# Kernel optimization log

Hardware: AMD Instinct MI355X
Metric: run time of the kernel (lower is better)

The kernel has to match this reference:

```python
import jax, jax.numpy as jnp
import numpy as np
from math import sqrt

DIM, RANK = 1024, 32
B, S = 4, 4096

def setup_inputs() -> dict:
    key = jax.random.key(0)
    kx, kq, kk, kv = jax.random.split(key, 4)
    # xavier_uniform bounds
    bq = sqrt(6.0 / (RANK + DIM))
    bv = sqrt(6.0 / (DIM + DIM))
    return {
        "x": jax.random.normal(kx, (B, S, DIM), dtype=jnp.float32),
        "Q": jax.random.uniform(kq, (RANK, DIM), jnp.float32, -bq, bq),
        "K": jax.random.uniform(kk, (RANK, DIM), jnp.float32, -bq, bq),
        "VO": jax.random.uniform(kv, (DIM, DIM), jnp.float32, -bv, bv),
    }

def reference(x, Q, K, VO):
    d = x.shape[-1]
    # low-rank projections: [b,t,r] each (avoid materializing QK^T [d,d] or 4-way einsum blowup)
    xq = jnp.einsum('btd,rd->btr', x, Q)
    xk = jnp.einsum('bud,rd->bur', x, K)
    scores = jnp.einsum('btr,bur->btu', xq, xk) / sqrt(d)
    attn = jax.nn.softmax(scores, axis=2)
    # value aggregation then output projection
    ctx = jnp.einsum('btu,bud->btd', attn, x)
    return jnp.einsum('btd,de->bte', ctx, VO)
```

## Files before the change

### kernel.cpp

```cpp
#include <hip/hip_runtime.h>
#include <hip/hip_bf16.h>

#define DIM  1024
#define RANK 32
#define BATCH 4
#define SEQ  4096
#define MTOT (BATCH * SEQ)

typedef short bf16x8 __attribute__((ext_vector_type(8)));
typedef float f32x4 __attribute__((ext_vector_type(4)));
typedef float f32x16 __attribute__((ext_vector_type(16)));
typedef unsigned short ushort8v __attribute__((ext_vector_type(8)));
typedef unsigned int uint2v __attribute__((ext_vector_type(2)));

__device__ inline unsigned short f2bf(float f) {
    union { float f; unsigned int u; } v; v.f = f;
    return (unsigned short)((v.u + 0x7FFFu + ((v.u >> 16) & 1u)) >> 16);
}

__device__ inline unsigned int pk_bf16(float a, float b) {
    __hip_bfloat162 h = __float22bfloat162_rn(make_float2(a, b));
    unsigned int u; __builtin_memcpy(&u, &h, 4);
    return u;
}

__device__ inline void gl_lds16(const unsigned short* g, unsigned short* l) {
    __builtin_amdgcn_global_load_lds(
        (const __attribute__((address_space(1))) unsigned int*)g,
        (__attribute__((address_space(3))) unsigned int*)l, 16, 0, 0);
}

__global__ __launch_bounds__(256) void k_cvt_qk(const float* __restrict__ Q,
                                                const float* __restrict__ K,
                                                unsigned short* __restrict__ wqk) {
    int i = blockIdx.x * 256 + threadIdx.x;
    int row = i >> 10, col = i & 1023;
    const float SC = 0.045084220027779984f;
    float v = (row < RANK) ? Q[row * DIM + col] * SC : K[(row - RANK) * DIM + col];
    wqk[i] = f2bf(v);
}

__global__ __launch_bounds__(256) void k_transpose_cvt(const float* __restrict__ in,
                                                       unsigned short* __restrict__ out,
                                                       int R, int C) {
    __shared__ float tile[64][65];
    const int tid = threadIdx.x;
    const int c0 = blockIdx.x * 64, r0 = blockIdx.y * 64;
    {
        int c = (tid & 15) * 4;
#pragma unroll
        for (int i = 0; i < 4; ++i) {
            int r = (tid >> 4) + i * 16;
            f32x4 v = *(const f32x4*)(in + (size_t)(r0 + r) * C + c0 + c);
            tile[r][c + 0] = v[0]; tile[r][c + 1] = v[1];
            tile[r][c + 2] = v[2]; tile[r][c + 3] = v[3];
        }
    }
    __syncthreads();
    {
        int r = (tid & 15) * 4;
#pragma unroll
        for (int i = 0; i < 4; ++i) {
            int c = (tid >> 4) + i * 16;
            unsigned short o0 = f2bf(tile[r + 0][c]), o1 = f2bf(tile[r + 1][c]);
            unsigned short o2 = f2bf(tile[r + 2][c]), o3 = f2bf(tile[r + 3][c]);
            unsigned short* p = out + (size_t)(c0 + c) * R + r0 + r;
            p[0] = o0; p[1] = o1; p[2] = o2; p[3] = o3;
        }
    }
}

__global__ __launch_bounds__(256) void k_xbf(const float* __restrict__ x,
                                             unsigned short* __restrict__ xbf) {
    size_t i = ((size_t)blockIdx.x * 256 + threadIdx.x) * 8;
    f32x4 v0 = *(const f32x4*)(x + i);
    f32x4 v1 = *(const f32x4*)(x + i + 4);
    ushort8v o;
    o[0] = f2bf(v0[0]); o[1] = f2bf(v0[1]); o[2] = f2bf(v0[2]); o[3] = f2bf(v0[3]);
    o[4] = f2bf(v1[0]); o[5] = f2bf(v1[1]); o[6] = f2bf(v1[2]); o[7] = f2bf(v1[3]);
    *(ushort8v*)(xbf + i) = o;
}

__global__ __launch_bounds__(256) void k_proj(const unsigned short* __restrict__ xbf,
                                              const unsigned short* __restrict__ wqk,
                                              unsigned short* __restrict__ xqk) {
    __shared__ __align__(16) unsigned short a_lds[128 * 32];
    __shared__ __align__(16) unsigned short w_lds[64 * 32];
    const int tid = threadIdx.x;
    const int w = tid >> 6, lane = tid & 63, l15 = lane & 15, quad = lane >> 4;
    const int wm = w & 1, wn = w >> 1;
    const int rowbase = blockIdx.x * 128;

    f32x4 acc[4][2];
#pragma unroll
    for (int mt = 0; mt < 4; ++mt)
#pragma unroll
        for (int nt = 0; nt < 2; ++nt) acc[mt][nt] = (f32x4){0.f, 0.f, 0.f, 0.f};

    const unsigned short* Ab = xbf + (size_t)(rowbase + w * 32 + (lane >> 2)) * DIM + (lane & 3) * 8;
    const unsigned short* Wb = wqk + (size_t)(w * 16 + (lane >> 2)) * DIM + (lane & 3) * 8;

    for (int k0 = 0; k0 < DIM; k0 += 32) {
        gl_lds16(Ab + k0, &a_lds[(w * 32) * 32]);
        gl_lds16(Ab + (size_t)16 * DIM + k0, &a_lds[(w * 32 + 16) * 32]);
        gl_lds16(Wb + k0, &w_lds[(w * 16) * 32]);
        __syncthreads();
        bf16x8 am[4], bn[2];
#pragma unroll
        for (int mt = 0; mt < 4; ++mt)
            am[mt] = *(const bf16x8*)&a_lds[(wm * 64 + mt * 16 + l15) * 32 + quad * 8];
#pragma unroll
        for (int nt = 0; nt < 2; ++nt)
            bn[nt] = *(const bf16x8*)&w_lds[(wn * 32 + nt * 16 + l15) * 32 + quad * 8];
#pragma unroll
        for (int mt = 0; mt < 4; ++mt)
#pragma unroll
            for (int nt = 0; nt < 2; ++nt)
                acc[mt][nt] = __builtin_amdgcn_mfma_f32_16x16x32_bf16(am[mt], bn[nt], acc[mt][nt], 0, 0, 0);
        __syncthreads();
    }
#pragma unroll
    for (int mt = 0; mt < 4; ++mt)
#pragma unroll
        for (int nt = 0; nt < 2; ++nt)
#pragma unroll
            for (int r = 0; r < 4; ++r) {
                int grow = rowbase + wm * 64 + mt * 16 + quad * 4 + r;
                xqk[(size_t)grow * 64 + wn * 32 + nt * 16 + l15] = f2bf(acc[mt][nt][r]);
            }
}

__global__ __launch_bounds__(512, 4) void k_xvo(const unsigned short* __restrict__ vot,
                                                const unsigned short* __restrict__ xbf,
                                                unsigned short* __restrict__ xvoT) {
    __shared__ __align__(16) unsigned short a_lds[128 * 64];
    __shared__ __align__(16) unsigned short b_lds[256 * 64];
    const int tid = threadIdx.x;
    const int w = tid >> 6, lane = tid & 63, l31 = lane & 31, half = lane >> 5;
    const int wm = w & 1, wn = w >> 1;
    const int ubase = blockIdx.x * 256;
    const int ebase = blockIdx.y * 128;
    const int b = blockIdx.z;

    f32x16 acc[2][2];
#pragma unroll
    for (int at = 0; at < 2; ++at)
#pragma unroll
        for (int bt = 0; bt < 2; ++bt)
#pragma unroll
            for (int i = 0; i < 16; ++i) acc[at][bt][i] = 0.f;

    const int sub = lane >> 3;
    const int g = (lane & 7) ^ (sub & 7);
    const int Ra = w * 16 + sub;
    const int Rb = w * 32 + sub;
    const unsigned short* Ap = vot + (size_t)(ebase + Ra) * DIM + g * 8;
    const unsigned short* Bp = xbf + (size_t)(b * SEQ + ubase + Rb) * DIM + g * 8;

    for (int k0 = 0; k0 < DIM; k0 += 64) {
#pragma unroll
        for (int c = 0; c < 2; ++c)
            gl_lds16(Ap + (size_t)(c * 8) * DIM + k0, &a_lds[(w * 16 + c * 8) * 64]);
#pragma unroll
        for (int c = 0; c < 4; ++c)
            gl_lds16(Bp + (size_t)(c * 8) * DIM + k0, &b_lds[(w * 32 + c * 8) * 64]);
        __syncthreads();

        const int abase = (wm * 64 + l31) * 64;
        const int bbase = (wn * 64 + l31) * 64;
#pragma unroll
        for (int ks = 0; ks < 4; ++ks) {
            const int soff = ((ks * 2 + half) ^ (l31 & 7)) * 8;
            bf16x8 a0 = *(const bf16x8*)&a_lds[abase + soff];
            bf16x8 a1 = *(const bf16x8*)&a_lds[abase + 2048 + soff];
            bf16x8 b0 = *(const bf16x8*)&b_lds[bbase + soff];
            bf16x8 b1 = *(const bf16x8*)&b_lds[bbase + 2048 + soff];
            acc[0][0] = __builtin_amdgcn_mfma_f32_32x32x16_bf16(a0, b0, acc[0][0], 0, 0, 0);
            acc[0][1] = __builtin_amdgcn_mfma_f32_32x32x16_bf16(a0, b1, acc[0][1], 0, 0, 0);
            acc[1][0] = __builtin_amdgcn_mfma_f32_32x32x16_bf16(a1, b0, acc[1][0], 0, 0, 0);
            acc[1][1] = __builtin_amdgcn_mfma_f32_32x32x16_bf16(a1, b1, acc[1][1], 0, 0, 0);
        }
        __syncthreads();
    }
#pragma unroll
    for (int at = 0; at < 2; ++at)
#pragma unroll
        for (int bt = 0; bt < 2; ++bt)
#pragma unroll
            for (int reg = 0; reg < 16; ++reg) {
                int lr = wm * 64 + at * 32 + (reg & 3) + 8 * (reg >> 2) + 4 * half;
                int u = ubase + wn * 64 + bt * 32 + l31;
                xvoT[(size_t)(b * DIM + ebase + lr) * SEQ + u] = f2bf(acc[at][bt][reg]);
            }
}

__global__ __launch_bounds__(512, 4) void k_spv(const unsigned short* __restrict__ xqk,
                                                const unsigned short* __restrict__ xvoT,
                                                float* __restrict__ out) {
    __shared__ __align__(16) unsigned short p_lds[128 * 64];
    __shared__ __align__(16) unsigned short b_lds[256 * 64];
    __shared__ float denp[8][32];
    __shared__ float rden[128];
    const int tid = threadIdx.x;
    const int w = tid >> 6, lane = tid & 63, l31 = lane & 31, half = lane >> 5;
    const int wm = w & 1, wn = w >> 1;
    const int uu = w & 1, qq = w >> 1;

    const int p = blockIdx.x;
    const int xcd = p & 7, t0 = p >> 3;
    const int rowtile = xcd * 16 + (t0 >> 2);
    const int etile = t0 & 3;
    const int rowbase = rowtile * 128;
    const int ebase = etile * 256;
    const int b = rowbase >> 12;

    const unsigned short* xqp = xqk + (size_t)(rowbase + qq * 32 + l31) * 64 + half * 8;
    const bf16x8 bq0 = *(const bf16x8*)(xqp);
    const bf16x8 bq1 = *(const bf16x8*)(xqp + 16);

    const unsigned short* xkp = xqk + (size_t)(b * SEQ + uu * 32 + l31) * 64 + 32 + half * 8;

    f32x16 acc[2][2];
#pragma unroll
    for (int at = 0; at < 2; ++at)
#pragma unroll
        for (int bt = 0; bt < 2; ++bt)
#pragma unroll
            for (int i = 0; i < 16; ++i) acc[at][bt][i] = 0.f;

    const int sub = lane >> 3;
    const int g8 = (lane & 7) ^ (sub & 7);
    const unsigned short* Bp = xvoT + (size_t)(b * DIM + ebase + w * 32 + sub) * SEQ + g8 * 8;
    auto stageB = [&](int k0) {
#pragma unroll
        for (int c = 0; c < 4; ++c)
            gl_lds16(Bp + (size_t)(c * 8) * SEQ + k0, &b_lds[(w * 32 + c * 8) * 64]);
    };

    const int NT = SEQ / 64;
    float dacc = 0.f;
    const int pbase = (qq * 32 + l31) * 64 + half * 4;

    stageB(0);
    bf16x8 kA0 = *(const bf16x8*)(xkp);
    bf16x8 kA1 = *(const bf16x8*)(xkp + 16);
    bf16x8 kB0, kB1;

    for (int t = 0; t < NT; ++t) {
        f32x16 sc;
#pragma unroll
        for (int i = 0; i < 16; ++i) sc[i] = 0.f;
        sc = __builtin_amdgcn_mfma_f32_32x32x16_bf16(kA0, bq0, sc, 0, 0, 0);
        sc = __builtin_amdgcn_mfma_f32_32x32x16_bf16(kA1, bq1, sc, 0, 0, 0);
#pragma unroll
        for (int g = 0; g < 4; ++g) {
            float e0 = exp2f(sc[4 * g + 0]), e1 = exp2f(sc[4 * g + 1]);
            float e2 = exp2f(sc[4 * g + 2]), e3 = exp2f(sc[4 * g + 3]);
            dacc += (e0 + e1) + (e2 + e3);
            uint2v dw; dw[0] = pk_bf16(e0, e1); dw[1] = pk_bf16(e2, e3);
            *(uint2v*)&p_lds[pbase + (((uu * 4 + g) ^ (l31 & 7)) * 8)] = dw;
        }
        asm volatile("s_waitcnt lgkmcnt(0)" ::: "memory");
        asm volatile("s_waitcnt vmcnt(0)" ::: "memory");
        __builtin_amdgcn_s_barrier();
        asm volatile("" ::: "memory");

        {
            const unsigned short* nx = xkp + (size_t)((t + 1 < NT) ? (t + 1) : t) * 4096;
            kB0 = *(const bf16x8*)(nx);
            kB1 = *(const bf16x8*)(nx + 16);
        }

        const int abase = (wm * 64 + l31) * 64;
        const int bbase = (wn * 64 + l31) * 64;
        __builtin_amdgcn_s_setprio(1);
#pragma unroll
        for (int ks = 0; ks < 4; ++ks) {
            const int soff = ((ks * 2 + half) ^ (l31 & 7)) * 8;
            bf16x8 a0 = *(const bf16x8*)&p_lds[abase + soff];
            bf16x8 a1 = *(const bf16x8*)&p_lds[abase + 2048 + soff];
            bf16x8 b0 = *(const bf16x8*)&b_lds[bbase + soff];
            bf16x8 b1 = *(const bf16x8*)&b_lds[bbase + 2048 + soff];
            acc[0][0] = __builtin_amdgcn_mfma_f32_32x32x16_bf16(a0, b0, acc[0][0], 0, 0, 0);
            acc[0][1] = __builtin_amdgcn_mfma_f32_32x32x16_bf16(a0, b1, acc[0][1], 0, 0, 0);
            acc[1][0] = __builtin_amdgcn_mfma_f32_32x32x16_bf16(a1, b0, acc[1][0], 0, 0, 0);
            acc[1][1] = __builtin_amdgcn_mfma_f32_32x32x16_bf16(a1, b1, acc[1][1], 0, 0, 0);
        }
        __builtin_amdgcn_s_setprio(0);
        asm volatile("s_waitcnt lgkmcnt(0)" ::: "memory");
        __builtin_amdgcn_s_barrier();
        asm volatile("" ::: "memory");

        if (t + 1 < NT) stageB((t + 1) * 64);
        kA0 = kB0; kA1 = kB1;
    }

    dacc += __shfl_xor(dacc, 32);
    if (half == 0) denp[w][l31] = dacc;
    __syncthreads();
    if (tid < 128)
        rden[tid] = 1.0f / (denp[(tid >> 5) * 2][tid & 31] + denp[(tid >> 5) * 2 + 1][tid & 31]);
    __syncthreads();

#pragma unroll
    for (int at = 0; at < 2; ++at)
#pragma unroll
        for (int bt = 0; bt < 2; ++bt)
#pragma unroll
            for (int reg = 0; reg < 16; ++reg) {
                int lr = wm * 64 + at * 32 + (reg & 3) + 8 * (reg >> 2) + 4 * half;
                int e = ebase + wn * 64 + bt * 32 + l31;
                out[(size_t)(rowbase + lr) * DIM + e] = acc[at][bt][reg] * rden[lr];
            }
}

extern "C" void kernel_launch(void* const* d_in, const int* in_sizes, int n_in,
                              void* d_out, int out_size, void* d_ws, size_t ws_size,
                              hipStream_t stream) {
    const float* x  = (const float*)d_in[0];
    const float* Q  = (const float*)d_in[1];
    const float* K  = (const float*)d_in[2];
    const float* VO = (const float*)d_in[3];
    float* out = (float*)d_out;

    char* ws = (char*)d_ws;
    unsigned short* wqk  = (unsigned short*)(ws + 0);
    unsigned short* vot  = (unsigned short*)(ws + 131072);
    unsigned short* xqk  = (unsigned short*)(ws + 2228224);
    unsigned short* xbf  = (unsigned short*)(ws + 4325376);
    unsigned short* xvoT = (unsigned short*)(ws + 37879808);

    k_cvt_qk<<<256, 256, 0, stream>>>(Q, K, wqk);
    k_transpose_cvt<<<dim3(16, 16, 1), 256, 0, stream>>>(VO, vot, 1024, 1024);
    k_xbf<<<8192, 256, 0, stream>>>(x, xbf);
    k_proj<<<128, 256, 0, stream>>>(xbf, wqk, xqk);
    k_xvo<<<dim3(16, 8, BATCH), 512, 0, stream>>>(vot, xbf, xvoT);
    k_spv<<<dim3(512, 1, 1), 512, 0, stream>>>(xqk, xvoT, out);
}
```

Before: 341.9 us.

## Software-pipeline score/exp computation with PV MFMA using double-buffered P tile

Double-buffers the probability tile in LDS so the scores MFMA and exp2 for tile t+1 are computed while the PV MFMAs for tile t run, instead of serially before them. The first tile's scores are computed in a prologue. The s_setprio hints are removed. B staging now waits on vmcnt right after issue and adds a second barrier per iteration, which exposes global-load latency that the old schedule partly hid behind the score computation.

```diff
diff --git a/kernel.cpp b/kernel.cpp
--- a/kernel.cpp
+++ b/kernel.cpp
@@ -197,7 +197,7 @@
 __global__ __launch_bounds__(512, 4) void k_spv(const unsigned short* __restrict__ xqk,
                                                 const unsigned short* __restrict__ xvoT,
                                                 float* __restrict__ out) {
-    __shared__ __align__(16) unsigned short p_lds[128 * 64];
+    __shared__ __align__(16) unsigned short p_lds[2][128 * 64];
     __shared__ __align__(16) unsigned short b_lds[256 * 64];
     __shared__ float denp[8][32];
     __shared__ float rden[128];
@@ -242,43 +242,52 @@
     const int pbase = (qq * 32 + l31) * 64 + half * 4;
 
     stageB(0);
-    bf16x8 kA0 = *(const bf16x8*)(xkp);
-    bf16x8 kA1 = *(const bf16x8*)(xkp + 16);
-    bf16x8 kB0, kB1;
-
-    for (int t = 0; t < NT; ++t) {
+    bf16x8 kCur0 = *(const bf16x8*)(xkp);
+    bf16x8 kCur1 = *(const bf16x8*)(xkp + 16);
+    {
         f32x16 sc;
 #pragma unroll
         for (int i = 0; i < 16; ++i) sc[i] = 0.f;
-        sc = __builtin_amdgcn_mfma_f32_32x32x16_bf16(kA0, bq0, sc, 0, 0, 0);
-        sc = __builtin_amdgcn_mfma_f32_32x32x16_bf16(kA1, bq1, sc, 0, 0, 0);
+        sc = __builtin_amdgcn_mfma_f32_32x32x16_bf16(kCur0, bq0, sc, 0, 0, 0);
+        sc = __builtin_amdgcn_mfma_f32_32x32x16_bf16(kCur1, bq1, sc, 0, 0, 0);
 #pragma unroll
         for (int g = 0; g < 4; ++g) {
             float e0 = exp2f(sc[4 * g + 0]), e1 = exp2f(sc[4 * g + 1]);
             float e2 = exp2f(sc[4 * g + 2]), e3 = exp2f(sc[4 * g + 3]);
             dacc += (e0 + e1) + (e2 + e3);
             uint2v dw; dw[0] = pk_bf16(e0, e1); dw[1] = pk_bf16(e2, e3);
-            *(uint2v*)&p_lds[pbase + (((uu * 4 + g) ^ (l31 & 7)) * 8)] = dw;
-        }
-        asm volatile("s_waitcnt lgkmcnt(0)" ::: "memory");
-        asm volatile("s_waitcnt vmcnt(0)" ::: "memory");
-        __builtin_amdgcn_s_barrier();
-        asm volatile("" ::: "memory");
-
-        {
-            const unsigned short* nx = xkp + (size_t)((t + 1 < NT) ? (t + 1) : t) * 4096;
-            kB0 = *(const bf16x8*)(nx);
-            kB1 = *(const bf16x8*)(nx + 16);
-        }
-
+            *(uint2v*)&p_lds[0][pbase + (((uu * 4 + g) ^ (l31 & 7)) * 8)] = dw;
+        }
+    }
+    {
+        const unsigned short* nx = xkp + 4096;
+        kCur0 = *(const bf16x8*)(nx);
+        kCur1 = *(const bf16x8*)(nx + 16);
+    }
+    asm volatile("s_waitcnt lgkmcnt(0)" ::: "memory");
+    asm volatile("s_waitcnt vmcnt(0)" ::: "memory");
+    __builtin_amdgcn_s_barrier();
+    asm volatile("" ::: "memory");
+
+    bf16x8 kNext0 = kCur0, kNext1 = kCur1;
+    for (int t = 0; t < NT; ++t) {
+        const bool more = (t + 1 < NT);
+        f32x16 sc;
+#pragma unroll
+        for (int i = 0; i < 16; ++i) sc[i] = 0.f;
+        if (more) {
+            sc = __builtin_amdgcn_mfma_f32_32x32x16_bf16(kCur0, bq0, sc, 0, 0, 0);
+            sc = __builtin_amdgcn_mfma_f32_32x32x16_bf16(kCur1, bq1, sc, 0, 0, 0);
+        }
+
+        const unsigned short* pl = p_lds[t & 1];
         const int abase = (wm * 64 + l31) * 64;
         const int bbase = (wn * 64 + l31) * 64;
-        __builtin_amdgcn_s_setprio(1);
 #pragma unroll
         for (int ks = 0; ks < 4; ++ks) {
             const int soff = ((ks * 2 + half) ^ (l31 & 7)) * 8;
-            bf16x8 a0 = *(const bf16x8*)&p_lds[abase + soff];
-            bf16x8 a1 = *(const bf16x8*)&p_lds[abase + 2048 + soff];
+            bf16x8 a0 = *(const bf16x8*)&pl[abase + soff];
+            bf16x8 a1 = *(const bf16x8*)&pl[abase + 2048 + soff];
             bf16x8 b0 = *(const bf16x8*)&b_lds[bbase + soff];
             bf16x8 b1 = *(const bf16x8*)&b_lds[bbase + 2048 + soff];
             acc[0][0] = __builtin_amdgcn_mfma_f32_32x32x16_bf16(a0, b0, acc[0][0], 0, 0, 0);
@@ -286,13 +295,32 @@
             acc[1][0] = __builtin_amdgcn_mfma_f32_32x32x16_bf16(a1, b0, acc[1][0], 0, 0, 0);
             acc[1][1] = __builtin_amdgcn_mfma_f32_32x32x16_bf16(a1, b1, acc[1][1], 0, 0, 0);
         }
-        __builtin_amdgcn_s_setprio(0);
+
+        if (more) {
+#pragma unroll
+            for (int g = 0; g < 4; ++g) {
+                float e0 = exp2f(sc[4 * g + 0]), e1 = exp2f(sc[4 * g + 1]);
+                float e2 = exp2f(sc[4 * g + 2]), e3 = exp2f(sc[4 * g + 3]);
+                dacc += (e0 + e1) + (e2 + e3);
+                uint2v dw; dw[0] = pk_bf16(e0, e1); dw[1] = pk_bf16(e2, e3);
+                *(uint2v*)&p_lds[(t + 1) & 1][pbase + (((uu * 4 + g) ^ (l31 & 7)) * 8)] = dw;
+            }
+            const unsigned short* nx = xkp + (size_t)((t + 2 < NT) ? (t + 2) : (t + 1)) * 4096;
+            kNext0 = *(const bf16x8*)(nx);
+            kNext1 = *(const bf16x8*)(nx + 16);
+        }
+
         asm volatile("s_waitcnt lgkmcnt(0)" ::: "memory");
         __builtin_amdgcn_s_barrier();
         asm volatile("" ::: "memory");
 
-        if (t + 1 < NT) stageB((t + 1) * 64);
-        kA0 = kB0; kA1 = kB1;
+        if (more) {
+            stageB((t + 1) * 64);
+            asm volatile("s_waitcnt vmcnt(0)" ::: "memory");
+        }
+        __builtin_amdgcn_s_barrier();
+        asm volatile("" ::: "memory");
+        kCur0 = kNext0; kCur1 = kNext1;
     }
 
     dacc += __shfl_xor(dacc, 32);
```

Result: slower. 363.5 us (+6.3%).

## Warp-specialize attention kernel into producer and MFMA consumer waves with double buffering

Applied to the files above, without the earlier changes.

Splits the eight waves of k_spv into four producer waves and four consumer waves. Producers compute scores, exponentials and the P tile and stage the xvoT tile into double-buffered LDS. Consumers only run the P·V MFMAs, each holding a larger 64x128 accumulator. The aim is to overlap softmax and global loads with matrix work, at the cost of doubled LDS, more accumulator registers and occupancy lowered to 2 blocks per CU. Barrier counts must match exactly across the two roles.

```diff
diff --git a/kernel.cpp b/kernel.cpp
--- a/kernel.cpp
+++ b/kernel.cpp
@@ -194,17 +194,14 @@
             }
 }
 
-__global__ __launch_bounds__(512, 4) void k_spv(const unsigned short* __restrict__ xqk,
+__global__ __launch_bounds__(512, 2) void k_spv(const unsigned short* __restrict__ xqk,
                                                 const unsigned short* __restrict__ xvoT,
                                                 float* __restrict__ out) {
-    __shared__ __align__(16) unsigned short p_lds[128 * 64];
-    __shared__ __align__(16) unsigned short b_lds[256 * 64];
-    __shared__ float denp[8][32];
+    __shared__ __align__(16) unsigned short p_lds[2][128 * 64];
+    __shared__ __align__(16) unsigned short b_lds[2][256 * 64];
     __shared__ float rden[128];
     const int tid = threadIdx.x;
     const int w = tid >> 6, lane = tid & 63, l31 = lane & 31, half = lane >> 5;
-    const int wm = w & 1, wn = w >> 1;
-    const int uu = w & 1, qq = w >> 1;
 
     const int p = blockIdx.x;
     const int xcd = p & 7, t0 = p >> 3;
@@ -214,104 +211,132 @@
     const int ebase = etile * 256;
     const int b = rowbase >> 12;
 
-    const unsigned short* xqp = xqk + (size_t)(rowbase + qq * 32 + l31) * 64 + half * 8;
-    const bf16x8 bq0 = *(const bf16x8*)(xqp);
-    const bf16x8 bq1 = *(const bf16x8*)(xqp + 16);
-
-    const unsigned short* xkp = xqk + (size_t)(b * SEQ + uu * 32 + l31) * 64 + 32 + half * 8;
-
-    f32x16 acc[2][2];
-#pragma unroll
-    for (int at = 0; at < 2; ++at)
-#pragma unroll
-        for (int bt = 0; bt < 2; ++bt)
-#pragma unroll
-            for (int i = 0; i < 16; ++i) acc[at][bt][i] = 0.f;
-
+    const int NT = SEQ / 64;
     const int sub = lane >> 3;
     const int g8 = (lane & 7) ^ (sub & 7);
-    const unsigned short* Bp = xvoT + (size_t)(b * DIM + ebase + w * 32 + sub) * SEQ + g8 * 8;
-    auto stageB = [&](int k0) {
-#pragma unroll
-        for (int c = 0; c < 4; ++c)
-            gl_lds16(Bp + (size_t)(c * 8) * SEQ + k0, &b_lds[(w * 32 + c * 8) * 64]);
-    };
-
-    const int NT = SEQ / 64;
-    float dacc = 0.f;
-    const int pbase = (qq * 32 + l31) * 64 + half * 4;
-
-    stageB(0);
-    bf16x8 kA0 = *(const bf16x8*)(xkp);
-    bf16x8 kA1 = *(const bf16x8*)(xkp + 16);
-    bf16x8 kB0, kB1;
-
-    for (int t = 0; t < NT; ++t) {
-        f32x16 sc;
-#pragma unroll
-        for (int i = 0; i < 16; ++i) sc[i] = 0.f;
-        sc = __builtin_amdgcn_mfma_f32_32x32x16_bf16(kA0, bq0, sc, 0, 0, 0);
-        sc = __builtin_amdgcn_mfma_f32_32x32x16_bf16(kA1, bq1, sc, 0, 0, 0);
-#pragma unroll
-        for (int g = 0; g < 4; ++g) {
-            float e0 = exp2f(sc[4 * g + 0]), e1 = exp2f(sc[4 * g + 1]);
-            float e2 = exp2f(sc[4 * g + 2]), e3 = exp2f(sc[4 * g + 3]);
-            dacc += (e0 + e1) + (e2 + e3);
-            uint2v dw; dw[0] = pk_bf16(e0, e1); dw[1] = pk_bf16(e2, e3);
-            *(uint2v*)&p_lds[pbase + (((uu * 4 + g) ^ (l31 & 7)) * 8)] = dw;
-        }
-        asm volatile("s_waitcnt lgkmcnt(0)" ::: "memory");
-        asm volatile("s_waitcnt vmcnt(0)" ::: "memory");
+
+    if (w < 4) {
+        const int pw = w;
+        const unsigned short* xqp = xqk + (size_t)(rowbase + pw * 32 + l31) * 64 + half * 8;
+        const bf16x8 bq0 = *(const bf16x8*)(xqp);
+        const bf16x8 bq1 = *(const bf16x8*)(xqp + 16);
+        const unsigned short* xkp = xqk + (size_t)(b * SEQ + l31) * 64 + 32 + half * 8;
+        const unsigned short* BpP = xvoT + (size_t)(b * DIM + ebase + pw * 64 + sub) * SEQ + g8 * 8;
+        const int pbase = (pw * 32 + l31) * 64 + half * 4;
+        float dacc = 0.f;
+        bf16x8 kc0[2], kc1[2];
+
+        auto load_k = [&](int tt) {
+#pragma unroll
+            for (int uu = 0; uu < 2; ++uu) {
+                const unsigned short* nx = xkp + (size_t)uu * 2048 + (size_t)tt * 4096;
+                kc0[uu] = *(const bf16x8*)(nx);
+                kc1[uu] = *(const bf16x8*)(nx + 16);
+            }
+        };
+        auto stage_b = [&](int buf, int tt) {
+            unsigned short* bl = b_lds[buf];
+#pragma unroll
+            for (int c = 0; c < 8; ++c)
+                gl_lds16(BpP + (size_t)(c * 8) * SEQ + tt * 64, &bl[(pw * 64 + c * 8) * 64]);
+        };
+        auto score_into = [&](int buf) {
+#pragma unroll
+            for (int uu = 0; uu < 2; ++uu) {
+                f32x16 sc;
+#pragma unroll
+                for (int i = 0; i < 16; ++i) sc[i] = 0.f;
+                sc = __builtin_amdgcn_mfma_f32_32x32x16_bf16(kc0[uu], bq0, sc, 0, 0, 0);
+                sc = __builtin_amdgcn_mfma_f32_32x32x16_bf16(kc1[uu], bq1, sc, 0, 0, 0);
+#pragma unroll
+                for (int g = 0; g < 4; ++g) {
+                    float e0 = exp2f(sc[4 * g + 0]), e1 = exp2f(sc[4 * g + 1]);
+                    float e2 = exp2f(sc[4 * g + 2]), e3 = exp2f(sc[4 * g + 3]);
+                    dacc += (e0 + e1) + (e2 + e3);
+                    uint2v dw; dw[0] = pk_bf16(e0, e1); dw[1] = pk_bf16(e2, e3);
+                    *(uint2v*)&p_lds[buf][pbase + (((uu * 4 + g) ^ (l31 & 7)) * 8)] = dw;
+                }
+            }
+        };
+
+        stage_b(0, 0);
+        load_k(0);
+        score_into(0);
+        load_k(1);
+        asm volatile("s_waitcnt vmcnt(0) lgkmcnt(0)" ::: "memory");
         __builtin_amdgcn_s_barrier();
         asm volatile("" ::: "memory");
 
-        {
-            const unsigned short* nx = xkp + (size_t)((t + 1 < NT) ? (t + 1) : t) * 4096;
-            kB0 = *(const bf16x8*)(nx);
-            kB1 = *(const bf16x8*)(nx + 16);
-        }
-
-        const int abase = (wm * 64 + l31) * 64;
-        const int bbase = (wn * 64 + l31) * 64;
-        __builtin_amdgcn_s_setprio(1);
-#pragma unroll
-        for (int ks = 0; ks < 4; ++ks) {
-            const int soff = ((ks * 2 + half) ^ (l31 & 7)) * 8;
-            bf16x8 a0 = *(const bf16x8*)&p_lds[abase + soff];
-            bf16x8 a1 = *(const bf16x8*)&p_lds[abase + 2048 + soff];
-            bf16x8 b0 = *(const bf16x8*)&b_lds[bbase + soff];
-            bf16x8 b1 = *(const bf16x8*)&b_lds[bbase + 2048 + soff];
-            acc[0][0] = __builtin_amdgcn_mfma_f32_32x32x16_bf16(a0, b0, acc[0][0], 0, 0, 0);
-            acc[0][1] = __builtin_amdgcn_mfma_f32_32x32x16_bf16(a0, b1, acc[0][1], 0, 0, 0);
-            acc[1][0] = __builtin_amdgcn_mfma_f32_32x32x16_bf16(a1, b0, acc[1][0], 0, 0, 0);
-            acc[1][1] = __builtin_amdgcn_mfma_f32_32x32x16_bf16(a1, b1, acc[1][1], 0, 0, 0);
-        }
-        __builtin_amdgcn_s_setprio(0);
-        asm volatile("s_waitcnt lgkmcnt(0)" ::: "memory");
+        for (int t = 0; t < NT; ++t) {
+            if (t + 1 < NT) {
+                stage_b((t + 1) & 1, t + 1);
+                score_into((t + 1) & 1);
+                load_k((t + 2 < NT) ? (t + 2) : (t + 1));
+                asm volatile("s_waitcnt vmcnt(0) lgkmcnt(0)" ::: "memory");
+            }
+            __builtin_amdgcn_s_barrier();
+            asm volatile("" ::: "memory");
+        }
+
+        dacc += __shfl_xor(dacc, 32);
+        if (half == 0) rden[pw * 32 + l31] = 1.0f / dacc;
+        __syncthreads();
+    } else {
+        const int cw = w - 4;
+        const int cm = cw & 1, cn = cw >> 1;
+        f32x16 acc[2][4];
+#pragma unroll
+        for (int at = 0; at < 2; ++at)
+#pragma unroll
+            for (int bt = 0; bt < 4; ++bt)
+#pragma unroll
+                for (int i = 0; i < 16; ++i) acc[at][bt][i] = 0.f;
+
         __builtin_amdgcn_s_barrier();
         asm volatile("" ::: "memory");
 
-        if (t + 1 < NT) stageB((t + 1) * 64);
-        kA0 = kB0; kA1 = kB1;
-    }
-
-    dacc += __shfl_xor(dacc, 32);
-    if (half == 0) denp[w][l31] = dacc;
-    __syncthreads();
-    if (tid < 128)
-        rden[tid] = 1.0f / (denp[(tid >> 5) * 2][tid & 31] + denp[(tid >> 5) * 2 + 1][tid & 31]);
-    __syncthreads();
-
-#pragma unroll
-    for (int at = 0; at < 2; ++at)
-#pragma unroll
-        for (int bt = 0; bt < 2; ++bt)
-#pragma unroll
-            for (int reg = 0; reg < 16; ++reg) {
-                int lr = wm * 64 + at * 32 + (reg & 3) + 8 * (reg >> 2) + 4 * half;
-                int e = ebase + wn * 64 + bt * 32 + l31;
-                out[(size_t)(rowbase + lr) * DIM + e] = acc[at][bt][reg] * rden[lr];
-            }
+        const int abase = (cm * 64 + l31) * 64;
+        const int bbase = (cn * 128 + l31) * 64;
+        for (int t = 0; t < NT; ++t) {
+            const unsigned short* pl = p_lds[t & 1];
+            const unsigned short* bl = b_lds[t & 1];
+            __builtin_amdgcn_s_setprio(1);
+#pragma unroll
+            for (int ks = 0; ks < 4; ++ks) {
+                const int soff = ((ks * 2 + half) ^ (l31 & 7)) * 8;
+                bf16x8 a0 = *(const bf16x8*)&pl[abase + soff];
+                bf16x8 a1 = *(const bf16x8*)&pl[abase + 2048 + soff];
+                bf16x8 b0 = *(const bf16x8*)&bl[bbase + soff];
+                bf16x8 b1 = *(const bf16x8*)&bl[bbase + 2048 + soff];
+                bf16x8 b2 = *(const bf16x8*)&bl[bbase + 4096 + soff];
+                bf16x8 b3 = *(const bf16x8*)&bl[bbase + 6144 + soff];
+                acc[0][0] = __builtin_amdgcn_mfma_f32_32x32x16_bf16(a0, b0, acc[0][0], 0, 0, 0);
+                acc[0][1] = __builtin_amdgcn_mfma_f32_32x32x16_bf16(a0, b1, acc[0][1], 0, 0, 0);
+                acc[0][2] = __builtin_amdgcn_mfma_f32_32x32x16_bf16(a0, b2, acc[0][2], 0, 0, 0);
+                acc[0][3] = __builtin_amdgcn_mfma_f32_32x32x16_bf16(a0, b3, acc[0][3], 0, 0, 0);
+                acc[1][0] = __builtin_amdgcn_mfma_f32_32x32x16_bf16(a1, b0, acc[1][0], 0, 0, 0);
+                acc[1][1] = __builtin_amdgcn_mfma_f32_32x32x16_bf16(a1, b1, acc[1][1], 0, 0, 0);
+                acc[1][2] = __builtin_amdgcn_mfma_f32_32x32x16_bf16(a1, b2, acc[1][2], 0, 0, 0);
+                acc[1][3] = __builtin_amdgcn_mfma_f32_32x32x16_bf16(a1, b3, acc[1][3], 0, 0, 0);
+            }
+            __builtin_amdgcn_s_setprio(0);
+            asm volatile("s_waitcnt lgkmcnt(0)" ::: "memory");
+            __builtin_amdgcn_s_barrier();
+            asm volatile("" ::: "memory");
+        }
+        __syncthreads();
+
+#pragma unroll
+        for (int at = 0; at < 2; ++at)
+#pragma unroll
+            for (int bt = 0; bt < 4; ++bt)
+#pragma unroll
+                for (int reg = 0; reg < 16; ++reg) {
+                    int lr = cm * 64 + at * 32 + (reg & 3) + 8 * (reg >> 2) + 4 * half;
+                    int e = ebase + cn * 128 + bt * 32 + l31;
+                    out[(size_t)(rowbase + lr) * DIM + e] = acc[at][bt][reg] * rden[lr];
+                }
+    }
 }
 
 extern "C" void kernel_launch(void* const* d_in, const int* in_sizes, int n_in,
```

New measurement: 382.0 us. 1.12x slower.
